# Optimization experiments

Hardware: AMD Instinct MI355X
Metric: run time of the kernel (lower is better)

The kernel has to match this reference:

```python
import jax, jax.numpy as jnp
import numpy as np

OUT_FEATURES = 4096
IN_FEATURES = 4096
K = 4096
BLOCK_SIZE = 8
NUM_BLOCKS = OUT_FEATURES * IN_FEATURES // BLOCK_SIZE  # 2,097,152
ORIGINAL_NUMEL = OUT_FEATURES * IN_FEATURES


def setup_inputs() -> dict:
    key = jax.random.key(0)
    k1, k2, k3, k4 = jax.random.split(key, 4)
    x = jax.random.normal(k1, (4, 2048, IN_FEATURES), dtype=jnp.float32)
    codebook = jax.random.normal(k2, (K, BLOCK_SIZE), dtype=jnp.float32)
    indices = jax.random.randint(k3, (NUM_BLOCKS,), 0, K, dtype=jnp.int64)
    bias = jax.random.normal(k4, (OUT_FEATURES,), dtype=jnp.float32)
    return {"x": x, "codebook": codebook, "indices": indices, "bias": bias}


def reference(x, codebook, indices, bias):
    # Reconstruct weight from codebook: gather blocks, flatten, slice, reshape.
    reconstructed = codebook[indices]                      # [num_blocks, block_size]
    W = reconstructed.reshape(-1)[:ORIGINAL_NUMEL]
    W = W.reshape(OUT_FEATURES, IN_FEATURES)               # [out, in]
    # F.linear: x @ W^T + bias
    return jnp.einsum('bsi,oi->bso', x, W) + bias
```

## Files before the change

### kernel.cpp

```cpp
#include <hip/hip_runtime.h>
#include <stdint.h>


#define M_DIM 8192
#define N_DIM 4096
#define K_DIM 4096
#define BM 256
#define BN 256
#define BK 64
#define NT (K_DIM / BK)
#define NUM_W_BLOCKS 2097152
#define W_WGS (NUM_W_BLOCKS / 256)
#define X_WGS ((M_DIM * K_DIM / 4) / 256)

typedef __attribute__((ext_vector_type(8))) __bf16 bf16x8;
typedef __attribute__((ext_vector_type(4))) float floatx4;
typedef __attribute__((ext_vector_type(2))) unsigned int uintx2;

__device__ __forceinline__ unsigned int f2bf(float f) {
    unsigned int u = __builtin_bit_cast(unsigned int, f);
    u += 0x7fffu + ((u >> 16) & 1u);
    return u >> 16;
}

__global__ __launch_bounds__(256) void prep_kernel(
    const float* __restrict__ cb, const int* __restrict__ idx,
    uint4* __restrict__ W, const floatx4* __restrict__ x,
    uintx2* __restrict__ xb) {
    const int wg = blockIdx.x;
    if (wg < W_WGS) {
        const int b = wg * 256 + threadIdx.x;
        const int id = __builtin_nontemporal_load(idx + b);
        const float4* s = (const float4*)(cb + ((size_t)id << 3));
        const float4 a = s[0];
        const float4 c = s[1];
        uint4 o;
        o.x = f2bf(a.x) | (f2bf(a.y) << 16);
        o.y = f2bf(a.z) | (f2bf(a.w) << 16);
        o.z = f2bf(c.x) | (f2bf(c.y) << 16);
        o.w = f2bf(c.z) | (f2bf(c.w) << 16);
        W[b] = o;
    } else {
        const size_t t = (size_t)(wg - W_WGS) * 256 + threadIdx.x;
        const floatx4 a = __builtin_nontemporal_load(x + t);
        uintx2 o;
        o.x = f2bf(a.x) | (f2bf(a.y) << 16);
        o.y = f2bf(a.z) | (f2bf(a.w) << 16);
        xb[t] = o;
    }
}

__device__ __forceinline__ void async_copy16(const __bf16* g, __bf16* s) {
    __builtin_amdgcn_global_load_lds(
        (const __attribute__((address_space(1))) unsigned int*)(uintptr_t)g,
        (__attribute__((address_space(3))) unsigned int*)(uintptr_t)s,
        16, 0, 0);
}

#define STAGE(gsrc, arr, slotElems)                                        \
    do {                                                                   \
        async_copy16((gsrc), (arr) + (slotElems) + wave512);               \
        async_copy16((gsrc) + (size_t)128 * K_DIM,                         \
                     (arr) + (slotElems) + 4096 + wave512);                \
    } while (0)

__global__ __launch_bounds__(512, 2) void gemm_bt_kernel(
    const __bf16* __restrict__ A,
    const __bf16* __restrict__ B,
    const float* __restrict__ bias,
    float* __restrict__ C) {
    __shared__ __align__(16) __bf16 sA[4 * 8192];
    __shared__ __align__(16) __bf16 sB[4 * 8192];

    const int tid = threadIdx.x;
    const int wave = tid >> 6;
    const int lane = tid & 63;
    const int wr = wave >> 2;
    const int wc = wave & 3;

    const int flat = blockIdx.x;
    const int xcd = flat & 7;
    const int q = flat >> 3;
    const int half = q >> 5;
    const int sq = q & 31;
    const int m0 = ((xcd & 3) * 8 + half * 4 + (sq & 3)) * BM;
    const int n0 = ((xcd >> 2) * 8 + (sq >> 2)) * BN;

    const int srow = tid >> 2;
    const int schunk = ((tid & 3) ^ ((srow >> 1) & 3)) << 3;
    const __bf16* gA = A + (size_t)(m0 + srow) * K_DIM + schunk;
    const __bf16* gB = B + (size_t)(n0 + srow) * K_DIM + schunk;
    const int wave512 = wave << 9;

    const int fr = lane & 15;
    const int roff = fr * 32 + (((lane >> 4) ^ ((fr >> 1) & 3)) << 3);
    const int aBase = wr * 4096 + roff;
    const int bBase = wc * 2048 + roff;

    floatx4 acc[8][4] = {};

    STAGE(gA, sA, 0);
    STAGE(gB, sB, 0);
    STAGE(gA + 32, sA, 8192);
    STAGE(gB + 32, sB, 8192);
    STAGE(gA + 64, sA, 16384);
    STAGE(gB + 64, sB, 16384);
    asm volatile("s_waitcnt vmcnt(8)" ::: "memory");
    __builtin_amdgcn_s_barrier();

    for (int t = 0; t < NT; ++t) {
        const int cs = (t & 1) ? 16384 : 0;
        const int ns = cs ^ 16384;
        const __bf16* sA0 = sA + cs;
        const __bf16* sA1 = sA + cs + 8192;
        const __bf16* sB0 = sB + cs;
        const __bf16* sB1 = sB + cs + 8192;

        bf16x8 af0[4], af1[4], bfr[4];

        if (t + 1 < NT) {
            STAGE(gA + (size_t)(t + 1) * 64 + 32, sA, ns + 8192);
            STAGE(gB + (size_t)(t + 1) * 64 + 32, sB, ns + 8192);
        }
#pragma unroll
        for (int i = 0; i < 4; ++i)
            af0[i] = *(const bf16x8*)(sA0 + aBase + i * 512);
#pragma unroll
        for (int j = 0; j < 4; ++j)
            bfr[j] = *(const bf16x8*)(sB0 + bBase + j * 512);
#pragma unroll
        for (int i = 0; i < 4; ++i)
            af1[i] = *(const bf16x8*)(sA0 + aBase + 2048 + i * 512);
        __builtin_amdgcn_s_setprio(1);
#pragma unroll
        for (int i = 0; i < 4; ++i)
#pragma unroll
            for (int j = 0; j < 4; ++j)
                acc[i][j] = __builtin_amdgcn_mfma_f32_16x16x32_bf16(
                    af0[i], bfr[j], acc[i][j], 0, 0, 0);
#pragma unroll
        for (int i = 0; i < 4; ++i)
#pragma unroll
            for (int j = 0; j < 4; ++j)
                acc[i + 4][j] = __builtin_amdgcn_mfma_f32_16x16x32_bf16(
                    af1[i], bfr[j], acc[i + 4][j], 0, 0, 0);
        __builtin_amdgcn_s_setprio(0);
        if (t + 1 < NT)
            asm volatile("s_waitcnt vmcnt(8)" ::: "memory");
        else
            asm volatile("s_waitcnt vmcnt(0)" ::: "memory");
        __builtin_amdgcn_s_barrier();

        if (t + 2 < NT) {
            STAGE(gA + (size_t)(t + 2) * 64, sA, cs);
            STAGE(gB + (size_t)(t + 2) * 64, sB, cs);
        }
#pragma unroll
        for (int i = 0; i < 4; ++i)
            af0[i] = *(const bf16x8*)(sA1 + aBase + i * 512);
#pragma unroll
        for (int j = 0; j < 4; ++j)
            bfr[j] = *(const bf16x8*)(sB1 + bBase + j * 512);
#pragma unroll
        for (int i = 0; i < 4; ++i)
            af1[i] = *(const bf16x8*)(sA1 + aBase + 2048 + i * 512);
        __builtin_amdgcn_s_setprio(1);
#pragma unroll
        for (int i = 0; i < 4; ++i)
#pragma unroll
            for (int j = 0; j < 4; ++j)
                acc[i][j] = __builtin_amdgcn_mfma_f32_16x16x32_bf16(
                    af0[i], bfr[j], acc[i][j], 0, 0, 0);
#pragma unroll
        for (int i = 0; i < 4; ++i)
#pragma unroll
            for (int j = 0; j < 4; ++j)
                acc[i + 4][j] = __builtin_amdgcn_mfma_f32_16x16x32_bf16(
                    af1[i], bfr[j], acc[i + 4][j], 0, 0, 0);
        __builtin_amdgcn_s_setprio(0);
        if (t + 2 < NT)
            asm volatile("s_waitcnt vmcnt(8)" ::: "memory");
        else if (t + 1 < NT)
            asm volatile("s_waitcnt vmcnt(4)" ::: "memory");
        else
            asm volatile("s_waitcnt vmcnt(0)" ::: "memory");
        __builtin_amdgcn_s_barrier();
    }

    const int crow = (lane >> 4) * 4;
    const int ccol = lane & 15;
#pragma unroll
    for (int j = 0; j < 4; ++j) {
        const int n = n0 + wc * 64 + j * 16 + ccol;
        const float bv = bias[n];
#pragma unroll
        for (int i = 0; i < 8; ++i) {
            const int m = m0 + wr * 128 + i * 16 + crow;
            float* cp = C + (size_t)m * N_DIM + n;
#pragma unroll
            for (int r = 0; r < 4; ++r)
                __builtin_nontemporal_store(acc[i][j][r] + bv,
                                            cp + (size_t)r * N_DIM);
        }
    }
}

extern "C" void kernel_launch(void* const* d_in, const int* in_sizes, int n_in,
                              void* d_out, int out_size, void* d_ws, size_t ws_size,
                              hipStream_t stream) {
    const float* x    = (const float*)d_in[0];
    const float* cb   = (const float*)d_in[1];
    const int*   idx  = (const int*)d_in[2];
    const float* bias = (const float*)d_in[3];
    float* out = (float*)d_out;

    __bf16* Wb = (__bf16*)d_ws;
    __bf16* Xb = (__bf16*)((char*)d_ws + (size_t)N_DIM * K_DIM * sizeof(__bf16));

    prep_kernel<<<W_WGS + X_WGS, 256, 0, stream>>>(
        cb, idx, (uint4*)Wb, (const floatx4*)x, (uintx2*)Xb);

    dim3 grid(M_DIM / BM * (N_DIM / BN));
    gemm_bt_kernel<<<grid, 512, 0, stream>>>(Xb, Wb, bias, out);
}
```

Measured before the change: 460.5 us.

## Prefetch next half-tile LDS fragments into registers during MFMA compute

Restructures the GEMM main loop so the A/B register fragments for the next K half-tile are loaded from LDS while the current MFMAs run. Fragments are carried across loop iterations, and a prologue loads the first set. Global-load wait counts are tightened to vmcnt(4) so the staged data is guaranteed resident before the early LDS reads. This aims to hide LDS read latency behind matrix ops, at the cost of extra live vector registers under a 512-thread, 2-block launch bound.

```diff
diff --git a/kernel.cpp b/kernel.cpp
--- a/kernel.cpp
+++ b/kernel.cpp
@@ -98,6 +98,7 @@
     const int bBase = wc * 2048 + roff;
 
     floatx4 acc[8][4] = {};
+    bf16x8 fA[4], fB[4], fC[4];
 
     STAGE(gA, sA, 0);
     STAGE(gB, sB, 0);
@@ -105,18 +106,24 @@
     STAGE(gB + 32, sB, 8192);
     STAGE(gA + 64, sA, 16384);
     STAGE(gB + 64, sB, 16384);
-    asm volatile("s_waitcnt vmcnt(8)" ::: "memory");
+    asm volatile("s_waitcnt vmcnt(4)" ::: "memory");
     __builtin_amdgcn_s_barrier();
+#pragma unroll
+    for (int i = 0; i < 4; ++i)
+        fA[i] = *(const bf16x8*)(sA + aBase + i * 512);
+#pragma unroll
+    for (int j = 0; j < 4; ++j)
+        fB[j] = *(const bf16x8*)(sB + bBase + j * 512);
 
     for (int t = 0; t < NT; ++t) {
         const int cs = (t & 1) ? 16384 : 0;
         const int ns = cs ^ 16384;
-        const __bf16* sA0 = sA + cs;
-        const __bf16* sA1 = sA + cs + 8192;
-        const __bf16* sB0 = sB + cs;
-        const __bf16* sB1 = sB + cs + 8192;
-
-        bf16x8 af0[4], af1[4], bfr[4];
+        const __bf16* pA0 = sA + cs;
+        const __bf16* pB0 = sB + cs;
+        const __bf16* pA1 = sA + cs + 8192;
+        const __bf16* pB1 = sB + cs + 8192;
+        const __bf16* nA0 = sA + ns;
+        const __bf16* nB0 = sB + ns;
 
         if (t + 1 < NT) {
             STAGE(gA + (size_t)(t + 1) * 64 + 32, sA, ns + 8192);
@@ -124,29 +131,31 @@
         }
 #pragma unroll
         for (int i = 0; i < 4; ++i)
-            af0[i] = *(const bf16x8*)(sA0 + aBase + i * 512);
+            fC[i] = *(const bf16x8*)(pA0 + aBase + 2048 + i * 512);
+        __builtin_amdgcn_s_setprio(1);
+#pragma unroll
+        for (int i = 0; i < 4; ++i)
+#pragma unroll
+            for (int j = 0; j < 4; ++j)
+                acc[i][j] = __builtin_amdgcn_mfma_f32_16x16x32_bf16(
+                    fA[i], fB[j], acc[i][j], 0, 0, 0);
+        __builtin_amdgcn_s_setprio(0);
+#pragma unroll
+        for (int i = 0; i < 4; ++i)
+            fA[i] = *(const bf16x8*)(pA1 + aBase + i * 512);
+        __builtin_amdgcn_s_setprio(1);
+#pragma unroll
+        for (int i = 0; i < 4; ++i)
+#pragma unroll
+            for (int j = 0; j < 4; ++j)
+                acc[i + 4][j] = __builtin_amdgcn_mfma_f32_16x16x32_bf16(
+                    fC[i], fB[j], acc[i + 4][j], 0, 0, 0);
+        __builtin_amdgcn_s_setprio(0);
 #pragma unroll
         for (int j = 0; j < 4; ++j)
-            bfr[j] = *(const bf16x8*)(sB0 + bBase + j * 512);
-#pragma unroll
-        for (int i = 0; i < 4; ++i)
-            af1[i] = *(const bf16x8*)(sA0 + aBase + 2048 + i * 512);
-        __builtin_amdgcn_s_setprio(1);
-#pragma unroll
-        for (int i = 0; i < 4; ++i)
-#pragma unroll
-            for (int j = 0; j < 4; ++j)
-                acc[i][j] = __builtin_amdgcn_mfma_f32_16x16x32_bf16(
-                    af0[i], bfr[j], acc[i][j], 0, 0, 0);
-#pragma unroll
-        for (int i = 0; i < 4; ++i)
-#pragma unroll
-            for (int j = 0; j < 4; ++j)
-                acc[i + 4][j] = __builtin_amdgcn_mfma_f32_16x16x32_bf16(
-                    af1[i], bfr[j], acc[i + 4][j], 0, 0, 0);
-        __builtin_amdgcn_s_setprio(0);
+            fB[j] = *(const bf16x8*)(pB1 + bBase + j * 512);
         if (t + 1 < NT)
-            asm volatile("s_waitcnt vmcnt(8)" ::: "memory");
+            asm volatile("s_waitcnt vmcnt(4)" ::: "memory");
         else
             asm volatile("s_waitcnt vmcnt(0)" ::: "memory");
         __builtin_amdgcn_s_barrier();
@@ -157,30 +166,34 @@
         }
 #pragma unroll
         for (int i = 0; i < 4; ++i)
-            af0[i] = *(const bf16x8*)(sA1 + aBase + i * 512);
-#pragma unroll
-        for (int j = 0; j < 4; ++j)
-            bfr[j] = *(const bf16x8*)(sB1 + bBase + j * 512);
-#pragma unroll
-        for (int i = 0; i < 4; ++i)
-            af1[i] = *(const bf16x8*)(sA1 + aBase + 2048 + i * 512);
+            fC[i] = *(const bf16x8*)(pA1 + aBase + 2048 + i * 512);
         __builtin_amdgcn_s_setprio(1);
 #pragma unroll
         for (int i = 0; i < 4; ++i)
 #pragma unroll
             for (int j = 0; j < 4; ++j)
                 acc[i][j] = __builtin_amdgcn_mfma_f32_16x16x32_bf16(
-                    af0[i], bfr[j], acc[i][j], 0, 0, 0);
+                    fA[i], fB[j], acc[i][j], 0, 0, 0);
+        __builtin_amdgcn_s_setprio(0);
+        if (t + 1 < NT) {
+#pragma unroll
+            for (int i = 0; i < 4; ++i)
+                fA[i] = *(const bf16x8*)(nA0 + aBase + i * 512);
+        }
+        __builtin_amdgcn_s_setprio(1);
 #pragma unroll
         for (int i = 0; i < 4; ++i)
 #pragma unroll
             for (int j = 0; j < 4; ++j)
                 acc[i + 4][j] = __builtin_amdgcn_mfma_f32_16x16x32_bf16(
-                    af1[i], bfr[j], acc[i + 4][j], 0, 0, 0);
-        __builtin_amdgcn_s_setprio(0);
+                    fC[i], fB[j], acc[i + 4][j], 0, 0, 0);
+        __builtin_amdgcn_s_setprio(0);
+        if (t + 1 < NT) {
+#pragma unroll
+            for (int j = 0; j < 4; ++j)
+                fB[j] = *(const bf16x8*)(nB0 + bBase + j * 512);
+        }
         if (t + 2 < NT)
-            asm volatile("s_waitcnt vmcnt(8)" ::: "memory");
-        else if (t + 1 < NT)
             asm volatile("s_waitcnt vmcnt(4)" ::: "memory");
         else
             asm volatile("s_waitcnt vmcnt(0)" ::: "memory");
```

After: 457.0 us. About the same (-0.8%).

## Shrink GEMM tile to 256x128 with 4 waves and triple-buffered BK=32 pipeline

Applied to the files above, without the earlier changes.

Changes the GEMM workgroup from 512 threads on 256x256 tiles to 256 threads on 256x128 tiles with BK=32. LDS buffering moves from a double-buffer of two 32-wide halves to a rotating three-slot ring prefetched two steps ahead, with one barrier per K step. The block-to-tile mapping is redone for the doubled grid and keeps the XCD-aware grouping. The intent is higher occupancy and smaller LDS use, at the cost of less data reuse per tile and twice as many barriers per unit of K.

```diff
diff --git a/kernel.cpp b/kernel.cpp
--- a/kernel.cpp
+++ b/kernel.cpp
@@ -6,9 +6,11 @@
 #define N_DIM 4096
 #define K_DIM 4096
 #define BM 256
-#define BN 256
-#define BK 64
+#define BN 128
+#define BK 32
 #define NT (K_DIM / BK)
+#define AUNIT 8192
+#define BUNIT 4096
 #define NUM_W_BLOCKS 2097152
 #define W_WGS (NUM_W_BLOCKS / 256)
 #define X_WGS ((M_DIM * K_DIM / 4) / 256)
@@ -57,34 +59,43 @@
         16, 0, 0);
 }
 
-#define STAGE(gsrc, arr, slotElems)                                        \
+#define STAGE_A(koff, aoff)                                                \
     do {                                                                   \
-        async_copy16((gsrc), (arr) + (slotElems) + wave512);               \
-        async_copy16((gsrc) + (size_t)128 * K_DIM,                         \
-                     (arr) + (slotElems) + 4096 + wave512);                \
+        const __bf16* g_ = gA + (koff);                                    \
+        async_copy16(g_, sA + (aoff) + wave512);                           \
+        async_copy16(g_ + (size_t)64 * K_DIM, sA + (aoff) + 2048 + wave512); \
+        async_copy16(g_ + (size_t)128 * K_DIM, sA + (aoff) + 4096 + wave512); \
+        async_copy16(g_ + (size_t)192 * K_DIM, sA + (aoff) + 6144 + wave512); \
+    } while (0)
+#define STAGE_B(koff, boff)                                                \
+    do {                                                                   \
+        const __bf16* g_ = gB + (koff);                                    \
+        async_copy16(g_, sB + (boff) + wave512);                           \
+        async_copy16(g_ + (size_t)64 * K_DIM, sB + (boff) + 2048 + wave512); \
     } while (0)
 
-__global__ __launch_bounds__(512, 2) void gemm_bt_kernel(
+__global__ __launch_bounds__(256, 2) void gemm_bt_kernel(
     const __bf16* __restrict__ A,
     const __bf16* __restrict__ B,
     const float* __restrict__ bias,
     float* __restrict__ C) {
-    __shared__ __align__(16) __bf16 sA[4 * 8192];
-    __shared__ __align__(16) __bf16 sB[4 * 8192];
+    __shared__ __align__(16) __bf16 sA[3 * AUNIT];
+    __shared__ __align__(16) __bf16 sB[3 * BUNIT];
 
     const int tid = threadIdx.x;
     const int wave = tid >> 6;
     const int lane = tid & 63;
-    const int wr = wave >> 2;
-    const int wc = wave & 3;
+    const int wr = wave >> 1;
+    const int wc = wave & 1;
 
     const int flat = blockIdx.x;
     const int xcd = flat & 7;
     const int q = flat >> 3;
-    const int half = q >> 5;
-    const int sq = q & 31;
-    const int m0 = ((xcd & 3) * 8 + half * 4 + (sq & 3)) * BM;
-    const int n0 = ((xcd >> 2) * 8 + (sq >> 2)) * BN;
+    const int sq = q & 63;
+    const int mi = (xcd & 3) * 8 + (sq & 7);
+    const int ni = (xcd >> 2) * 16 + (q >> 6) * 8 + (sq >> 3);
+    const int m0 = mi * BM;
+    const int n0 = ni * BN;
 
     const int srow = tid >> 2;
     const int schunk = ((tid & 3) ^ ((srow >> 1) & 3)) << 3;
@@ -93,98 +104,53 @@
     const int wave512 = wave << 9;
 
     const int fr = lane & 15;
-    const int roff = fr * 32 + (((lane >> 4) ^ ((fr >> 1) & 3)) << 3);
-    const int aBase = wr * 4096 + roff;
-    const int bBase = wc * 2048 + roff;
+    const int phys8 = (((lane >> 4) ^ ((fr >> 1) & 3)) << 3);
+    const int aBase = (wr * 128 + fr) * 32 + phys8;
+    const int bBase = (wc * 64 + fr) * 32 + phys8;
 
     floatx4 acc[8][4] = {};
 
-    STAGE(gA, sA, 0);
-    STAGE(gB, sB, 0);
-    STAGE(gA + 32, sA, 8192);
-    STAGE(gB + 32, sB, 8192);
-    STAGE(gA + 64, sA, 16384);
-    STAGE(gB + 64, sB, 16384);
-    asm volatile("s_waitcnt vmcnt(8)" ::: "memory");
+    STAGE_A(0, 0);
+    STAGE_B(0, 0);
+    STAGE_A(32, AUNIT);
+    STAGE_B(32, BUNIT);
+    asm volatile("s_waitcnt vmcnt(6)" ::: "memory");
     __builtin_amdgcn_s_barrier();
 
+    int cur = 0, nxt = 1, nx2 = 2;
+
     for (int t = 0; t < NT; ++t) {
-        const int cs = (t & 1) ? 16384 : 0;
-        const int ns = cs ^ 16384;
-        const __bf16* sA0 = sA + cs;
-        const __bf16* sA1 = sA + cs + 8192;
-        const __bf16* sB0 = sB + cs;
-        const __bf16* sB1 = sB + cs + 8192;
+        if (t + 2 < NT) {
+            STAGE_A((t + 2) * BK, nx2 * AUNIT);
+            STAGE_B((t + 2) * BK, nx2 * BUNIT);
+        }
 
-        bf16x8 af0[4], af1[4], bfr[4];
-
-        if (t + 1 < NT) {
-            STAGE(gA + (size_t)(t + 1) * 64 + 32, sA, ns + 8192);
-            STAGE(gB + (size_t)(t + 1) * 64 + 32, sB, ns + 8192);
-        }
+        const __bf16* pA = sA + cur * AUNIT;
+        const __bf16* pB = sB + cur * BUNIT;
+        bf16x8 af[8], bf4[4];
 #pragma unroll
-        for (int i = 0; i < 4; ++i)
-            af0[i] = *(const bf16x8*)(sA0 + aBase + i * 512);
+        for (int i = 0; i < 8; ++i)
+            af[i] = *(const bf16x8*)(pA + aBase + i * 512);
 #pragma unroll
         for (int j = 0; j < 4; ++j)
-            bfr[j] = *(const bf16x8*)(sB0 + bBase + j * 512);
-#pragma unroll
-        for (int i = 0; i < 4; ++i)
-            af1[i] = *(const bf16x8*)(sA0 + aBase + 2048 + i * 512);
+            bf4[j] = *(const bf16x8*)(pB + bBase + j * 512);
+
         __builtin_amdgcn_s_setprio(1);
 #pragma unroll
-        for (int i = 0; i < 4; ++i)
+        for (int i = 0; i < 8; ++i)
 #pragma unroll
             for (int j = 0; j < 4; ++j)
                 acc[i][j] = __builtin_amdgcn_mfma_f32_16x16x32_bf16(
-                    af0[i], bfr[j], acc[i][j], 0, 0, 0);
-#pragma unroll
-        for (int i = 0; i < 4; ++i)
-#pragma unroll
-            for (int j = 0; j < 4; ++j)
-                acc[i + 4][j] = __builtin_amdgcn_mfma_f32_16x16x32_bf16(
-                    af1[i], bfr[j], acc[i + 4][j], 0, 0, 0);
+                    af[i], bf4[j], acc[i][j], 0, 0, 0);
         __builtin_amdgcn_s_setprio(0);
-        if (t + 1 < NT)
-            asm volatile("s_waitcnt vmcnt(8)" ::: "memory");
+
+        if (t + 2 < NT)
+            asm volatile("s_waitcnt vmcnt(6)" ::: "memory");
         else
             asm volatile("s_waitcnt vmcnt(0)" ::: "memory");
         __builtin_amdgcn_s_barrier();
 
-        if (t + 2 < NT) {
-            STAGE(gA + (size_t)(t + 2) * 64, sA, cs);
-            STAGE(gB + (size_t)(t + 2) * 64, sB, cs);
-        }
-#pragma unroll
-        for (int i = 0; i < 4; ++i)
-            af0[i] = *(const bf16x8*)(sA1 + aBase + i * 512);
-#pragma unroll
-        for (int j = 0; j < 4; ++j)
-            bfr[j] = *(const bf16x8*)(sB1 + bBase + j * 512);
-#pragma unroll
-        for (int i = 0; i < 4; ++i)
-            af1[i] = *(const bf16x8*)(sA1 + aBase + 2048 + i * 512);
-        __builtin_amdgcn_s_setprio(1);
-#pragma unroll
-        for (int i = 0; i < 4; ++i)
-#pragma unroll
-            for (int j = 0; j < 4; ++j)
-                acc[i][j] = __builtin_amdgcn_mfma_f32_16x16x32_bf16(
-                    af0[i], bfr[j], acc[i][j], 0, 0, 0);
-#pragma unroll
-        for (int i = 0; i < 4; ++i)
-#pragma unroll
-            for (int j = 0; j < 4; ++j)
-                acc[i + 4][j] = __builtin_amdgcn_mfma_f32_16x16x32_bf16(
-                    af1[i], bfr[j], acc[i + 4][j], 0, 0, 0);
-        __builtin_amdgcn_s_setprio(0);
-        if (t + 2 < NT)
-            asm volatile("s_waitcnt vmcnt(8)" ::: "memory");
-        else if (t + 1 < NT)
-            asm volatile("s_waitcnt vmcnt(4)" ::: "memory");
-        else
-            asm volatile("s_waitcnt vmcnt(0)" ::: "memory");
-        __builtin_amdgcn_s_barrier();
+        const int tmp = cur; cur = nxt; nxt = nx2; nx2 = tmp;
     }
 
     const int crow = (lane >> 4) * 4;
@@ -220,6 +186,6 @@
     prep_kernel<<<W_WGS + X_WGS, 256, 0, stream>>>(
         cb, idx, (uint4*)Wb, (const floatx4*)x, (uintx2*)Xb);
 
-    dim3 grid(M_DIM / BM * (N_DIM / BN));
-    gemm_bt_kernel<<<grid, 512, 0, stream>>>(Xb, Wb, bias, out);
+    dim3 grid((M_DIM / BM) * (N_DIM / BN));
+    gemm_bt_kernel<<<grid, 256, 0, stream>>>(Xb, Wb, bias, out);
 }
```

Result: slower. 477.9 us (+3.8%).
